# Kernel optimization log

Measured on AMD Instinct MI355X. Metric: run time of the kernel, lower is better.

Reference implementation:

```python
import jax, jax.numpy as jnp
import numpy as np

NUM_WIRES = 12
NUM_LAYERS = 3
BATCH = 8192
DIM = 2 ** NUM_WIRES


def _rx(theta):
    # RX(t) = [[cos(t/2), -i sin(t/2)], [-i sin(t/2), cos(t/2)]]; theta scalar or (B,)
    h = theta * 0.5
    c = jnp.cos(h).astype(jnp.complex64)
    s = (-1j) * jnp.sin(h).astype(jnp.complex64)
    return jnp.stack([jnp.stack([c, s], -1), jnp.stack([s, c], -1)], -2)


def _ry(theta):
    # RY(t) = [[cos(t/2), -sin(t/2)], [sin(t/2), cos(t/2)]]
    h = theta * 0.5
    c = jnp.cos(h)
    s = jnp.sin(h)
    m = jnp.stack([jnp.stack([c, -s], -1), jnp.stack([s, c], -1)], -2)
    return m.astype(jnp.complex64)


def _apply_1q(psi, mat, wire):
    # psi: (B, 2**n); pennylane wire 0 is most significant bit
    B = psi.shape[0]
    s = psi.reshape(B, 2 ** wire, 2, -1)
    if mat.ndim == 2:
        out = jnp.einsum('ij,bajc->baic', mat, s)
    else:  # per-sample gate, mat: (B, 2, 2)
        out = jnp.einsum('bij,bajc->baic', mat, s)
    return out.reshape(B, -1)


def _cnot(psi, control, target):
    B = psi.shape[0]
    a, b = (control, target) if control < target else (target, control)
    s = psi.reshape(B, 2 ** a, 2, 2 ** (b - a - 1), 2, -1)
    if control == a:
        # control on axis 2, flip target (axis 4) where control bit == 1
        s = s.at[:, :, 1].set(s[:, :, 1, :, ::-1])
    else:
        # control on axis 4, flip target (axis 2) where control bit == 1
        s = s.at[:, :, :, :, 1].set(s[:, :, ::-1, :, 1])
    return s.reshape(B, -1)


def _circuit(angles, weights):
    # angles: (B, n) per-sample input rotations; weights: (L, n, 2)
    B = angles.shape[0]
    n = NUM_WIRES
    psi = jnp.zeros((B, DIM), jnp.complex64).at[:, 0].set(1.0)
    for i in range(n):
        psi = _apply_1q(psi, _rx(angles[:, i]), i)
        psi = _apply_1q(psi, _ry(angles[:, i]), i)
    for l in range(NUM_LAYERS):
        for i in range(n):
            psi = _apply_1q(psi, _rx(weights[l, i, 0]), i)
            psi = _apply_1q(psi, _ry(weights[l, i, 1]), i)
        for i in range(n - 1):
            psi = _cnot(psi, i, i + 1)
        psi = _cnot(psi, n - 1, 0)
    probs = (psi.real ** 2 + psi.imag ** 2).reshape((B,) + (2,) * n)
    zs = []
    for i in range(n):
        other = tuple(j + 1 for j in range(n) if j != i)
        p = probs.sum(other)  # (B, 2)
        zs.append(p[:, 0] - p[:, 1])  # <Z_i> = P(0) - P(1)
    return jnp.stack(zs, -1)  # (B, n)


def setup_inputs() -> dict:
    key = jax.random.key(0)
    ks = jax.random.split(key, 5)
    return {
        'state_real': jax.random.normal(ks[0], (BATCH, DIM), jnp.float32),
        'state_imag': jax.random.normal(ks[1], (BATCH, DIM), jnp.float32),
        'weights': jax.random.normal(ks[2], (NUM_LAYERS, NUM_WIRES, 2), jnp.float32),
        'head_w': jax.random.normal(ks[3], (1, NUM_WIRES), jnp.float32) / np.sqrt(NUM_WIRES).astype(np.float32),
        'head_b': jax.random.normal(ks[4], (1,), jnp.float32),
    }


def reference(state_real, state_imag, weights, head_w, head_b):
    angles = jnp.arctan2(state_imag[:, :NUM_WIRES], state_real[:, :NUM_WIRES])  # (B, n)
    q = _circuit(angles, weights)  # (B, n)
    return (q @ head_w.T + head_b).squeeze(-1)  # (B,)
```

## Files before the change

### kernel.cpp

```cpp
#include <hip/hip_runtime.h>

typedef __fp16 h2v __attribute__((ext_vector_type(2)));
typedef _Float16 f16x8 __attribute__((ext_vector_type(8)));
typedef float f32x4 __attribute__((ext_vector_type(4)));

#define BLK 256
#define BATCH 8192

struct M12 { unsigned r[12]; };

constexpr M12 mp_matrix() {
  M12 m{};
  for (int p = 0; p <= 10; ++p) m.r[p] = (0xFFFu >> p) << p;
  m.r[11] = 0x7FFu;
  return m;
}
constexpr M12 MP = mp_matrix();

constexpr unsigned mv(const M12 m, unsigned v) {
  unsigned y = 0;
  for (int p = 0; p < 12; ++p)
    y |= (unsigned)(__builtin_popcount(m.r[p] & v) & 1) << p;
  return y;
}
constexpr M12 mmul(const M12 a, const M12 b) {
  M12 c{};
  for (int p = 0; p < 12; ++p) {
    unsigned acc = 0;
    for (int q = 0; q < 12; ++q)
      if ((a.r[p] >> q) & 1u) acc ^= b.r[q];
    c.r[p] = acc;
  }
  return c;
}
constexpr M12 minv(const M12 a0) {
  unsigned a[12] = {}, v[12] = {};
  for (int i = 0; i < 12; ++i) { a[i] = a0.r[i]; v[i] = 1u << i; }
  for (int c = 0; c < 12; ++c) {
    int piv = c;
    while (!((a[piv] >> c) & 1u)) ++piv;
    unsigned ta = a[piv], tv = v[piv];
    a[piv] = a[c]; v[piv] = v[c]; a[c] = ta; v[c] = tv;
    for (int r2 = 0; r2 < 12; ++r2)
      if (r2 != c && ((a[r2] >> c) & 1u)) { a[r2] ^= a[c]; v[r2] ^= v[c]; }
  }
  M12 out{};
  for (int i = 0; i < 12; ++i) out.r[i] = v[i];
  return out;
}
constexpr unsigned colq(const M12 m, int q) {
  unsigned c = 0;
  for (int p = 0; p < 12; ++p) c |= ((m.r[p] >> q) & 1u) << p;
  return c;
}
constexpr M12 from_cols(const unsigned (&c)[12]) {
  M12 m{};
  for (int p = 0; p < 12; ++p) {
    unsigned row = 0;
    for (int j = 0; j < 12; ++j) row |= ((c[j] >> p) & 1u) << j;
    m.r[p] = row;
  }
  return m;
}
constexpr M12 mk_id() { M12 m{}; for (int p = 0; p < 12; ++p) m.r[p] = 1u << p; return m; }
constexpr M12 MID = mk_id();
constexpr M12 MPI = minv(MP);

constexpr bool meq(const M12 a, const M12 b) {
  for (int p = 0; p < 12; ++p) if (a.r[p] != b.r[p]) return false;
  return true;
}
static_assert(meq(mmul(MP, MPI), MID), "P inverse");

struct Frame { M12 A, Ai; };
constexpr Frame FID{MID, MID};
constexpr Frame absorb(const Frame f) { return Frame{ mmul(MP, f.A), mmul(f.Ai, MPI) }; }
constexpr Frame apply_tau(const Frame f, const M12 t) {
  return Frame{ mmul(f.A, minv(t)), mmul(t, f.Ai) };
}

struct SSet { unsigned S[12]; };

constexpr int bankrank(const unsigned* v, int n) {
  unsigned basis[5] = {};
  int r = 0;
  for (int i = 0; i < n; ++i) {
    unsigned x = v[i] & 31u;
    for (int b = 4; b >= 0; --b) {
      if (!((x >> b) & 1u)) continue;
      if (basis[b]) x ^= basis[b];
      else { basis[b] = x; ++r; break; }
    }
  }
  return r;
}
constexpr bool ins_ech(unsigned (&e)[12], unsigned x) {
  for (int b = 11; b >= 0; --b) {
    if (!((x >> b) & 1u)) continue;
    if (e[b]) x ^= e[b];
    else { e[b] = x; return true; }
  }
  return false;
}
constexpr SSet build_S(const Frame f, const int* qs) {
  SSet s{};
  unsigned rows[4] = {};
  for (int i = 0; i < 4; ++i) {
    s.S[i] = colq(f.Ai, qs[i]);
    rows[i] = f.A.r[qs[i]];
  }
  unsigned R[4] = {rows[0], rows[1], rows[2], rows[3]};
  int pivcol[4] = {-1, -1, -1, -1};
  int nr = 0;
  for (int cc = 0; cc < 12 && nr < 4; ++cc) {
    int pr = -1;
    for (int r2 = nr; r2 < 4; ++r2) if ((R[r2] >> cc) & 1u) { pr = r2; break; }
    if (pr < 0) continue;
    unsigned tmp = R[nr]; R[nr] = R[pr]; R[pr] = tmp;
    for (int r2 = 0; r2 < 4; ++r2)
      if (r2 != nr && ((R[r2] >> cc) & 1u)) R[r2] ^= R[nr];
    pivcol[nr] = cc; ++nr;
  }
  unsigned nb[8] = {};
  int nc = 0;
  for (int j = 0; j < 12; ++j) {
    bool isp = false;
    for (int k = 0; k < nr; ++k) if (pivcol[k] == j) isp = true;
    if (isp) continue;
    unsigned v = 1u << j;
    for (int k = 0; k < nr; ++k) if ((R[k] >> j) & 1u) v |= 1u << pivcol[k];
    nb[nc] = v;
    ++nc;
  }
  unsigned pool[36] = {};
  int np = 0;
  for (int j = 0; j < 8; ++j) pool[np++] = nb[j];
  for (int j = 0; j < 8; ++j)
    for (int k = j + 1; k < 8; ++k) pool[np++] = nb[j] ^ nb[k];
  unsigned ech[12] = {};
  unsigned readset[5] = {};
  int nrs = 0;
  readset[nrs++] = s.S[0];
  for (int slot = 4; slot <= 7; ++slot) {
    int best = -1;
    unsigned bestc = 0;
    for (int c = 0; c < np; ++c) {
      unsigned tmp[12];
      for (int z = 0; z < 12; ++z) tmp[z] = ech[z];
      if (!ins_ech(tmp, pool[c])) continue;
      readset[nrs] = pool[c];
      const int rk = bankrank(readset, nrs + 1);
      if (rk > best) { best = rk; bestc = pool[c]; }
    }
    s.S[slot] = bestc;
    ins_ech(ech, bestc);
    readset[nrs++] = bestc;
  }
  const int rem[4] = {8, 9, 10, 11};
  for (int t = 0; t < 4; ++t) {
    for (int c = 0; c < np; ++c) {
      unsigned tmp[12];
      for (int z = 0; z < 12; ++z) tmp[z] = ech[z];
      if (!ins_ech(tmp, pool[c])) continue;
      s.S[rem[t]] = pool[c];
      ins_ech(ech, pool[c]);
      break;
    }
  }
  return s;
}
constexpr unsigned T4[4] = {8u, 4u, 2u, 1u};
constexpr M12 tau_of(const SSet s) {
  unsigned Sc[12], Dc[12];
  for (int i = 0; i < 12; ++i) {
    Sc[i] = s.S[i];
    Dc[i] = (i < 4) ? T4[i] : (1u << i);
  }
  return mmul(from_cols(Dc), minv(from_cols(Sc)));
}
constexpr int readrank_of(const SSet s) {
  unsigned v[5] = {s.S[0], s.S[4], s.S[5], s.S[6], s.S[7]};
  return bankrank(v, 5);
}
constexpr bool chk_group(const Frame f, const int* qs) {
  for (int i = 0; i < 4; ++i) if (colq(f.Ai, qs[i]) != T4[i]) return false;
  return true;
}

constexpr int QA[4] = {11, 10, 9, 8};
constexpr int QB[4] = {7, 6, 5, 4};
constexpr int QC[4] = {3, 2, 1, 0};

constexpr Frame F1  = absorb(FID);
constexpr SSet C0 = build_S(F1, QA);
constexpr M12  T0 = tau_of(C0);
constexpr Frame F2a = apply_tau(F1, T0);
constexpr SSet C1 = build_S(F2a, QB);
constexpr M12  T1 = tau_of(C1);
constexpr Frame F2b = apply_tau(F2a, T1);
constexpr SSet C2 = build_S(F2b, QC);
constexpr M12  T2 = tau_of(C2);
constexpr Frame F2c = apply_tau(F2b, T2);
constexpr Frame F3  = absorb(F2c);
constexpr SSet C3 = build_S(F3, QA);
constexpr M12  T3m = tau_of(C3);
constexpr Frame F3a = apply_tau(F3, T3m);
constexpr SSet C4 = build_S(F3a, QB);
constexpr M12  T4m = tau_of(C4);
constexpr Frame F3b = apply_tau(F3a, T4m);
constexpr SSet C5 = build_S(F3b, QC);
constexpr M12  T5m = tau_of(C5);
constexpr Frame F3c = apply_tau(F3b, T5m);
constexpr Frame F4  = absorb(F3c);

static_assert(chk_group(F2a, QA), "G2a");
static_assert(chk_group(F2b, QB), "G2b");
static_assert(chk_group(F2c, QC), "G2c");
static_assert(chk_group(F3a, QA), "G3a");
static_assert(chk_group(F3b, QB), "G3b");
static_assert(chk_group(F3c, QC), "G3c");
static_assert(F2a.A.r[11] == 8u && F2a.A.r[10] == 4u && F2a.A.r[9] == 2u && F2a.A.r[8] == 1u, "rows2a");
static_assert(F2b.A.r[7]  == 8u && F2b.A.r[6]  == 4u && F2b.A.r[5] == 2u && F2b.A.r[4] == 1u, "rows2b");
static_assert(F2c.A.r[3]  == 8u && F2c.A.r[2]  == 4u && F2c.A.r[1] == 2u && F2c.A.r[0] == 1u, "rows2c");
static_assert(F3a.A.r[11] == 8u && F3a.A.r[10] == 4u && F3a.A.r[9] == 2u && F3a.A.r[8] == 1u, "rows3a");
static_assert(F3b.A.r[7]  == 8u && F3b.A.r[6]  == 4u && F3b.A.r[5] == 2u && F3b.A.r[4] == 1u, "rows3b");
static_assert(F3c.A.r[3]  == 8u && F3c.A.r[2]  == 4u && F3c.A.r[1] == 2u && F3c.A.r[0] == 1u, "rows3c");
static_assert(readrank_of(C0) >= 3 && readrank_of(C1) >= 3 && readrank_of(C2) >= 3 &&
              readrank_of(C3) >= 3 && readrank_of(C4) >= 3 && readrank_of(C5) >= 3, "rr");

struct PT { unsigned rlb[5]; unsigned rwb[2]; unsigned ro[32]; };
constexpr PT mk_pt(const SSet s) {
  PT t{};
  t.rlb[0] = s.S[4]; t.rlb[1] = s.S[5]; t.rlb[2] = s.S[6]; t.rlb[3] = s.S[7];
  t.rlb[4] = s.S[0];
  t.rwb[0] = s.S[10]; t.rwb[1] = s.S[11];
  for (int m = 0; m < 4; ++m)
    for (int j = 0; j < 8; ++j)
      t.ro[(m << 3) | j] = ((m & 1) ? s.S[8] : 0u) ^ ((m & 2) ? s.S[9] : 0u) ^
                           ((j & 1) ? s.S[3] : 0u) ^ ((j & 2) ? s.S[2] : 0u) ^
                           ((j & 4) ? s.S[1] : 0u);
  return t;
}
constexpr PT RT[6] = { mk_pt(C0), mk_pt(C1), mk_pt(C2),
                       mk_pt(C3), mk_pt(C4), mk_pt(C5) };

template<int PI>
__device__ __forceinline__ unsigned rbase_of(const int lane, const int w) {
  unsigned rb = 0u;
  #pragma unroll
  for (int k = 0; k < 4; ++k) rb ^= ((lane >> k) & 1) ? RT[PI].rlb[k] : 0u;
  rb ^= ((lane >> 4) & 1) ? RT[PI].rlb[4] : 0u;
  rb ^= (w & 1) ? RT[PI].rwb[0] : 0u;
  rb ^= (w & 2) ? RT[PI].rwb[1] : 0u;
  return rb;
}

template<int PI>
__device__ __forceinline__ void do_pass(f32x4 (&D1)[4], f32x4 (&D2)[4],
                                        const unsigned* sb,
                                        const uint4 a1u, const uint4 a2u,
                                        const int lane, const int w,
                                        const unsigned sel) {
  const f16x8 A1f = __builtin_bit_cast(f16x8, a1u);
  const f16x8 A2f = __builtin_bit_cast(f16x8, a2u);
  const unsigned rb = rbase_of<PI>(lane, w);
  const f32x4 z4 = {0.f, 0.f, 0.f, 0.f};
  #pragma unroll
  for (int m = 0; m < 4; ++m) {
    unsigned amp[8];
    #pragma unroll
    for (int j = 0; j < 8; ++j)
      amp[j] = sb[rb ^ RT[PI].ro[(m << 3) | j]];
    uint4 bw;
    bw.x = __builtin_amdgcn_perm(amp[1], amp[0], sel);
    bw.y = __builtin_amdgcn_perm(amp[3], amp[2], sel);
    bw.z = __builtin_amdgcn_perm(amp[5], amp[4], sel);
    bw.w = __builtin_amdgcn_perm(amp[7], amp[6], sel);
    const f16x8 Bf = __builtin_bit_cast(f16x8, bw);
    D1[m] = __builtin_amdgcn_mfma_f32_16x16x32_f16(A1f, Bf, z4, 0, 0, 0);
    D2[m] = __builtin_amdgcn_mfma_f32_16x16x32_f16(A2f, Bf, z4, 0, 0, 0);
  }
}

__device__ __forceinline__ void write_state(const f32x4 (&D1)[4],
                                            const f32x4 (&D2)[4],
                                            unsigned* sb, const int lane,
                                            const int w) {
  const unsigned base = ((unsigned)w << 10) | ((unsigned)(lane & 15) << 4) |
                        ((unsigned)(lane >> 4) << 2);
  #pragma unroll
  for (int m = 0; m < 4; ++m) {
    uint4 v;
    v.x = __builtin_bit_cast(unsigned, __builtin_amdgcn_cvt_pkrtz(D1[m][0], D2[m][0]));
    v.y = __builtin_bit_cast(unsigned, __builtin_amdgcn_cvt_pkrtz(D1[m][1], D2[m][1]));
    v.z = __builtin_bit_cast(unsigned, __builtin_amdgcn_cvt_pkrtz(D1[m][2], D2[m][2]));
    v.w = __builtin_bit_cast(unsigned, __builtin_amdgcn_cvt_pkrtz(D1[m][3], D2[m][3]));
    *(uint4*)(sb + (base | ((unsigned)m << 8))) = v;
  }
}

__device__ __forceinline__ void gentry(const float4 g, const int rb,
                                       const int kb, float& re, float& im) {
  re = rb ? (kb ? g.x : g.z) : (kb ? -g.z : g.x);
  im = rb ? (kb ? -g.y : g.w) : (kb ? g.w : g.y);
}

__global__ __launch_bounds__(BLK) void amat_kernel(
    const float* __restrict__ wts, uint4* __restrict__ Am) {
  __shared__ float4 gt4[24];
  const int t = threadIdx.x;
  if (t < 24) {
    const int l = 1 + t / 12, i = t % 12;
    const float a  = wts[(l * 12 + i) * 2 + 0] * 0.5f;
    const float bb = wts[(l * 12 + i) * 2 + 1] * 0.5f;
    float sa, ca, sb2, cb;
    sincosf(a, &sa, &ca);
    sincosf(bb, &sb2, &cb);
    gt4[t] = make_float4(cb * ca, sb2 * sa, sb2 * ca, -cb * sa);
  }
  __syncthreads();
  #pragma unroll
  for (int rep = 0; rep < 3; ++rep) {
    const int idx = t + rep * BLK;
    const int pass = idx >> 7;
    const int mat  = (idx >> 6) & 1;
    const int lw   = idx & 63;
    const int r    = lw & 15;
    const int ks   = lw >> 4;
    const int imf  = ks >> 1;
    const float4 g0 = gt4[pass * 4 + 0];
    const float4 g1 = gt4[pass * 4 + 1];
    const float4 g2 = gt4[pass * 4 + 2];
    const float4 g3 = gt4[pass * 4 + 3];
    float b3r, b3i;
    gentry(g0, (r >> 3) & 1, ks & 1, b3r, b3i);
    float t2r[2], t2i[2];
    #pragma unroll
    for (int k2 = 0; k2 < 2; ++k2) {
      float cr, ci;
      gentry(g1, (r >> 2) & 1, k2, cr, ci);
      t2r[k2] = b3r * cr - b3i * ci;
      t2i[k2] = b3r * ci + b3i * cr;
    }
    float t1r[4], t1i[4];
    #pragma unroll
    for (int k2 = 0; k2 < 2; ++k2)
      #pragma unroll
      for (int k1 = 0; k1 < 2; ++k1) {
        float cr, ci;
        gentry(g2, (r >> 1) & 1, k1, cr, ci);
        t1r[k2 * 2 + k1] = t2r[k2] * cr - t2i[k2] * ci;
        t1i[k2 * 2 + k1] = t2r[k2] * ci + t2i[k2] * cr;
      }
    float ev[8];
    #pragma unroll
    for (int j = 0; j < 8; ++j) {
      float cr, ci;
      gentry(g3, r & 1, j & 1, cr, ci);
      const int h2 = j >> 1;
      const float er = t1r[h2] * cr - t1i[h2] * ci;
      const float ei = t1r[h2] * ci + t1i[h2] * cr;
      ev[j] = (mat == 0) ? (imf ? -ei : er) : (imf ? er : ei);
    }
    unsigned u[4];
    #pragma unroll
    for (int q = 0; q < 4; ++q) {
      const h2v pk = __builtin_amdgcn_cvt_pkrtz(ev[2 * q], ev[2 * q + 1]);
      u[q] = __builtin_bit_cast(unsigned, pk);
    }
    Am[(pass * 2 + mat) * 64 + lw] = make_uint4(u[0], u[1], u[2], u[3]);
  }
}

__global__ __launch_bounds__(BLK, 4) void qsim_kernel(
    const float* __restrict__ sr, const float* __restrict__ si,
    const float* __restrict__ wts, const float* __restrict__ hw,
    const float* __restrict__ hb, const uint4* __restrict__ Am,
    float* __restrict__ out) {
  __shared__ __align__(16) unsigned sbuf[2][4096];
  float4* qv = (float4*)(sbuf[1]);
  float* xacc = (float*)(sbuf[0]);

  const int t = threadIdx.x;
  const int lane = t & 63;
  const int w = t >> 6;
  const int s = blockIdx.x;

  uint4 A1u[6], A2u[6];
  #pragma unroll
  for (int p = 0; p < 6; ++p) {
    A1u[p] = Am[(p * 2 + 0) * 64 + lane];
    A2u[p] = Am[(p * 2 + 1) * 64 + lane];
  }

  if (t >= 64 && t < 76) {
    const int i = t - 64;
    const float ang = atan2f(si[(size_t)s * 4096 + i],
                             sr[(size_t)s * 4096 + i]) * 0.5f;
    float sn, cs;
    sincosf(ang, &sn, &cs);
    const float e0r = cs * cs, e0i = sn * sn, e1r = sn * cs, e1i = -sn * cs;
    const float a  = wts[i * 2 + 0] * 0.5f;
    const float bb = wts[i * 2 + 1] * 0.5f;
    float sa, ca, sb2, cb;
    sincosf(a, &sa, &ca);
    sincosf(bb, &sb2, &cb);
    const float g00r = cb * ca,  g00i = sb2 * sa, g01r = -sb2 * ca, g01i = -cb * sa;
    const float g10r = sb2 * ca, g10i = -cb * sa, g11r = cb * ca,   g11i = -sb2 * sa;
    const float q0r = g00r * e0r - g00i * e0i + g01r * e1r - g01i * e1i;
    const float q0i = g00r * e0i + g00i * e0r + g01r * e1i + g01i * e1r;
    const float q1r = g10r * e0r - g10i * e0i + g11r * e1r - g11i * e1i;
    const float q1i = g10r * e0i + g10i * e0r + g11r * e1i + g11i * e1r;
    qv[i] = make_float4(q0r, q0i, q1r, q1i);
  }
  __syncthreads();

  {
    const float4* q = qv;
    float Lr, Li;
    { const float4 q0 = q[0]; const int b0 = (w >> 1) & 1;
      Lr = b0 ? q0.z : q0.x; Li = b0 ? q0.w : q0.y; }
    { const float4 q1 = q[1]; const int b1 = w & 1;
      const float fr = b1 ? q1.z : q1.x, fi = b1 ? q1.w : q1.y;
      const float nr = Lr * fr - Li * fi, ni = Lr * fi + Li * fr;
      Lr = nr; Li = ni; }
    #pragma unroll
    for (int i = 2; i <= 7; ++i) {
      const float4 qq = q[i];
      const int bit = (lane >> (7 - i)) & 1;
      const float fr = bit ? qq.z : qq.x, fi = bit ? qq.w : qq.y;
      const float nr = Lr * fr - Li * fi, ni = Lr * fi + Li * fr;
      Lr = nr; Li = ni;
    }
    float LTr[4], LTi[4];
    { const float4 q8 = q[8], q9 = q[9];
      #pragma unroll
      for (int m = 0; m < 4; ++m) {
        const float xr2 = (m & 2) ? q8.z : q8.x, xi2 = (m & 2) ? q8.w : q8.y;
        const float yr = (m & 1) ? q9.z : q9.x, yi = (m & 1) ? q9.w : q9.y;
        const float tr = xr2 * yr - xi2 * yi, ti = xr2 * yi + xi2 * yr;
        LTr[m] = Lr * tr - Li * ti;
        LTi[m] = Lr * ti + Li * tr;
      } }
    float tbr[4], tbi[4];
    { const float4 qA = q[10], qB2 = q[11];
      #pragma unroll
      for (int m = 0; m < 4; ++m) {
        const float xr2 = (m & 2) ? qA.z : qA.x, xi2 = (m & 2) ? qA.w : qA.y;
        const float yr = (m & 1) ? qB2.z : qB2.x, yi = (m & 1) ? qB2.w : qB2.y;
        tbr[m] = xr2 * yr - xi2 * yi;
        tbi[m] = xr2 * yi + xi2 * yr;
      } }
    __syncthreads();
    const unsigned base = ((unsigned)w << 10) | ((unsigned)lane << 4);
    #pragma unroll
    for (int qq2 = 0; qq2 < 4; ++qq2) {
      uint4 v;
      unsigned* vp = &v.x;
      #pragma unroll
      for (int z = 0; z < 4; ++z) {
        const int l = qq2 * 4 + z;
        const float arl = LTr[l >> 2] * tbr[l & 3] - LTi[l >> 2] * tbi[l & 3];
        const float ail = LTr[l >> 2] * tbi[l & 3] + LTi[l >> 2] * tbr[l & 3];
        vp[z] = __builtin_bit_cast(unsigned, __builtin_amdgcn_cvt_pkrtz(arl, ail));
      }
      *(uint4*)(sbuf[0] + base + qq2 * 4) = v;
    }
  }
  __syncthreads();

  const unsigned sel = (lane & 32) ? 0x07060302u : 0x05040100u;
  f32x4 D1[4], D2[4];

  do_pass<0>(D1, D2, sbuf[0], A1u[0], A2u[0], lane, w, sel);
  write_state(D1, D2, sbuf[1], lane, w);
  __syncthreads();
  do_pass<1>(D1, D2, sbuf[1], A1u[1], A2u[1], lane, w, sel);
  write_state(D1, D2, sbuf[0], lane, w);
  __syncthreads();
  do_pass<2>(D1, D2, sbuf[0], A1u[2], A2u[2], lane, w, sel);
  write_state(D1, D2, sbuf[1], lane, w);
  __syncthreads();
  do_pass<3>(D1, D2, sbuf[1], A1u[3], A2u[3], lane, w, sel);
  write_state(D1, D2, sbuf[0], lane, w);
  __syncthreads();
  do_pass<4>(D1, D2, sbuf[0], A1u[4], A2u[4], lane, w, sel);
  write_state(D1, D2, sbuf[1], lane, w);
  __syncthreads();
  do_pass<5>(D1, D2, sbuf[1], A1u[5], A2u[5], lane, w, sel);

  const unsigned pbase = ((unsigned)w << 10) | ((unsigned)(lane & 15) << 4) |
                         ((unsigned)((lane >> 4) & 3) << 2);
  float hp[12];
  #pragma unroll
  for (int i = 0; i < 12; ++i) {
    const unsigned R = F4.A.r[11 - i];
    const float h = hw[i];
    hp[i] = (__popc(pbase & R & 0xCFCu) & 1) ? -h : h;
  }
  float c[16];
  #pragma unroll
  for (int v = 0; v < 16; ++v) c[v] = 0.f;
  #pragma unroll
  for (int i = 0; i < 12; ++i) {
    const unsigned R = F4.A.r[11 - i];
    const int mu = (int)((((R >> 8) & 3u) << 2) | (R & 3u));
    c[mu] += hp[i];
  }
  #pragma unroll
  for (int bb = 1; bb < 16; bb <<= 1)
    #pragma unroll
    for (int v = 0; v < 16; ++v)
      if (!(v & bb)) {
        const float x = c[v], y = c[v | bb];
        c[v] = x + y;
        c[v | bb] = x - y;
      }
  float acc = 0.f;
  #pragma unroll
  for (int m = 0; m < 4; ++m)
    #pragma unroll
    for (int r = 0; r < 4; ++r)
      acc += (D1[m][r] * D1[m][r] + D2[m][r] * D2[m][r]) * c[(m << 2) | r];
  #pragma unroll
  for (int off = 1; off < 64; off <<= 1) acc += __shfl_xor(acc, off, 64);

  __syncthreads();
  if (lane == 0) xacc[w] = acc;
  __syncthreads();
  if (t == 0) out[s] = xacc[0] + xacc[1] + xacc[2] + xacc[3] + hb[0];
}

extern "C" void kernel_launch(void* const* d_in, const int* in_sizes, int n_in,
                              void* d_out, int out_size, void* d_ws, size_t ws_size,
                              hipStream_t stream) {
  const float* sr  = (const float*)d_in[0];
  const float* si  = (const float*)d_in[1];
  const float* wts = (const float*)d_in[2];
  const float* hw  = (const float*)d_in[3];
  const float* hb  = (const float*)d_in[4];
  float* out = (float*)d_out;
  uint4* Am = (uint4*)d_ws;
  amat_kernel<<<1, BLK, 0, stream>>>(wts, Am);
  qsim_kernel<<<BATCH, BLK, 0, stream>>>(sr, si, wts, hw, hb, Am, out);
}
```

Before: 103.3 us.

## Add per-pass XOR bank swizzle to LDS state layout to cut conflicts

Introduces a compile-time searched XOR swizzle per pass that maps high address bits into bank-selecting bits, chosen to maximize the bank rank of the gather read pattern. Both writes of the state (initial fill and between passes) and the gathered reads apply the same swizzle, so each buffer is consistently permuted. The candidate selection for the basis also now prioritizes low-bit rank. The aim is fewer LDS bank conflicts in the strided amplitude gathers, at the cost of slightly more address XOR arithmetic.

```diff
diff --git a/kernel.cpp b/kernel.cpp
--- a/kernel.cpp
+++ b/kernel.cpp
@@ -81,11 +81,11 @@
 
 struct SSet { unsigned S[12]; };
 
-constexpr int bankrank(const unsigned* v, int n) {
+constexpr int rank_msk(const unsigned* v, int n, unsigned msk) {
   unsigned basis[5] = {};
   int r = 0;
   for (int i = 0; i < n; ++i) {
-    unsigned x = v[i] & 31u;
+    unsigned x = v[i] & msk;
     for (int b = 4; b >= 0; --b) {
       if (!((x >> b) & 1u)) continue;
       if (basis[b]) x ^= basis[b];
@@ -149,8 +149,9 @@
       for (int z = 0; z < 12; ++z) tmp[z] = ech[z];
       if (!ins_ech(tmp, pool[c])) continue;
       readset[nrs] = pool[c];
-      const int rk = bankrank(readset, nrs + 1);
-      if (rk > best) { best = rk; bestc = pool[c]; }
+      const int score = rank_msk(readset, nrs + 1, 3u) * 8 +
+                        rank_msk(readset, nrs + 1, 31u);
+      if (score > best) { best = score; bestc = pool[c]; }
     }
     s.S[slot] = bestc;
     ins_ech(ech, bestc);
@@ -178,13 +179,37 @@
   }
   return mmul(from_cols(Dc), minv(from_cols(Sc)));
 }
-constexpr int readrank_of(const SSet s) {
-  unsigned v[5] = {s.S[0], s.S[4], s.S[5], s.S[6], s.S[7]};
-  return bankrank(v, 5);
-}
 constexpr bool chk_group(const Frame f, const int* qs) {
   for (int i = 0; i < 4; ++i) if (colq(f.Ai, qs[i]) != T4[i]) return false;
   return true;
+}
+
+struct BSw { unsigned mk[7]; };
+constexpr unsigned bapp(const BSw& b, unsigned v) {
+  unsigned o = v;
+  for (int k = 0; k < 7; ++k)
+    if ((v >> (5 + k)) & 1u) o ^= b.mk[k];
+  return o;
+}
+constexpr int brank_read(const BSw& b, const SSet& s) {
+  unsigned v[5] = { bapp(b, s.S[0]), bapp(b, s.S[4]), bapp(b, s.S[5]),
+                    bapp(b, s.S[6]), bapp(b, s.S[7]) };
+  return rank_msk(v, 5, 31u);
+}
+constexpr BSw find_B(const SSet& s) {
+  BSw b{};
+  int best = brank_read(b, s);
+  for (int sw = 0; sw < 3; ++sw)
+    for (int k = 0; k < 7; ++k) {
+      unsigned bv = b.mk[k];
+      for (unsigned v = 0; v < 8; ++v) {
+        b.mk[k] = v << 2;
+        const int r = brank_read(b, s);
+        if (r > best) { best = r; bv = v << 2; }
+      }
+      b.mk[k] = bv;
+    }
+  return b;
 }
 
 constexpr int QA[4] = {11, 10, 9, 8};
@@ -225,24 +250,40 @@
 static_assert(F3a.A.r[11] == 8u && F3a.A.r[10] == 4u && F3a.A.r[9] == 2u && F3a.A.r[8] == 1u, "rows3a");
 static_assert(F3b.A.r[7]  == 8u && F3b.A.r[6]  == 4u && F3b.A.r[5] == 2u && F3b.A.r[4] == 1u, "rows3b");
 static_assert(F3c.A.r[3]  == 8u && F3c.A.r[2]  == 4u && F3c.A.r[1] == 2u && F3c.A.r[0] == 1u, "rows3c");
-static_assert(readrank_of(C0) >= 3 && readrank_of(C1) >= 3 && readrank_of(C2) >= 3 &&
-              readrank_of(C3) >= 3 && readrank_of(C4) >= 3 && readrank_of(C5) >= 3, "rr");
-
-struct PT { unsigned rlb[5]; unsigned rwb[2]; unsigned ro[32]; };
-constexpr PT mk_pt(const SSet s) {
+
+constexpr BSw B0 = find_B(C0);
+constexpr BSw B1 = find_B(C1);
+constexpr BSw B2 = find_B(C2);
+constexpr BSw B3 = find_B(C3);
+constexpr BSw B4 = find_B(C4);
+constexpr BSw B5 = find_B(C5);
+static_assert(brank_read(B0, C0) >= 3 && brank_read(B1, C1) >= 3 &&
+              brank_read(B2, C2) >= 3 && brank_read(B3, C3) >= 3 &&
+              brank_read(B4, C4) >= 3 && brank_read(B5, C5) >= 3, "rr");
+
+struct PT {
+  unsigned rlb[5]; unsigned rwb[2]; unsigned ro[32];
+  unsigned wlb[4]; unsigned wm[2]; unsigned wwb[2];
+};
+constexpr PT mk_pt(const SSet s, const BSw b) {
   PT t{};
-  t.rlb[0] = s.S[4]; t.rlb[1] = s.S[5]; t.rlb[2] = s.S[6]; t.rlb[3] = s.S[7];
-  t.rlb[4] = s.S[0];
-  t.rwb[0] = s.S[10]; t.rwb[1] = s.S[11];
+  t.rlb[0] = bapp(b, s.S[4]); t.rlb[1] = bapp(b, s.S[5]);
+  t.rlb[2] = bapp(b, s.S[6]); t.rlb[3] = bapp(b, s.S[7]);
+  t.rlb[4] = bapp(b, s.S[0]);
+  t.rwb[0] = bapp(b, s.S[10]); t.rwb[1] = bapp(b, s.S[11]);
   for (int m = 0; m < 4; ++m)
     for (int j = 0; j < 8; ++j)
-      t.ro[(m << 3) | j] = ((m & 1) ? s.S[8] : 0u) ^ ((m & 2) ? s.S[9] : 0u) ^
-                           ((j & 1) ? s.S[3] : 0u) ^ ((j & 2) ? s.S[2] : 0u) ^
-                           ((j & 4) ? s.S[1] : 0u);
+      t.ro[(m << 3) | j] = bapp(b,
+          ((m & 1) ? s.S[8] : 0u) ^ ((m & 2) ? s.S[9] : 0u) ^
+          ((j & 1) ? s.S[3] : 0u) ^ ((j & 2) ? s.S[2] : 0u) ^
+          ((j & 4) ? s.S[1] : 0u));
+  for (int k = 0; k < 4; ++k) t.wlb[k] = bapp(b, 1u << (4 + k));
+  t.wm[0] = bapp(b, 256u);  t.wm[1] = bapp(b, 512u);
+  t.wwb[0] = bapp(b, 1024u); t.wwb[1] = bapp(b, 2048u);
   return t;
 }
-constexpr PT RT[6] = { mk_pt(C0), mk_pt(C1), mk_pt(C2),
-                       mk_pt(C3), mk_pt(C4), mk_pt(C5) };
+constexpr PT RT[6] = { mk_pt(C0, B0), mk_pt(C1, B1), mk_pt(C2, B2),
+                       mk_pt(C3, B3), mk_pt(C4, B4), mk_pt(C5, B5) };
 
 template<int PI>
 __device__ __forceinline__ unsigned rbase_of(const int lane, const int w) {
@@ -282,20 +323,26 @@
   }
 }
 
+template<int PI>
 __device__ __forceinline__ void write_state(const f32x4 (&D1)[4],
                                             const f32x4 (&D2)[4],
                                             unsigned* sb, const int lane,
                                             const int w) {
-  const unsigned base = ((unsigned)w << 10) | ((unsigned)(lane & 15) << 4) |
-                        ((unsigned)(lane >> 4) << 2);
+  unsigned wb = (unsigned)((lane >> 4) << 2);
+  #pragma unroll
+  for (int k = 0; k < 4; ++k) wb ^= ((lane >> k) & 1) ? RT[PI].wlb[k] : 0u;
+  wb ^= (w & 1) ? RT[PI].wwb[0] : 0u;
+  wb ^= (w & 2) ? RT[PI].wwb[1] : 0u;
   #pragma unroll
   for (int m = 0; m < 4; ++m) {
+    const unsigned addr = wb ^ ((m & 1) ? RT[PI].wm[0] : 0u)
+                             ^ ((m & 2) ? RT[PI].wm[1] : 0u);
     uint4 v;
     v.x = __builtin_bit_cast(unsigned, __builtin_amdgcn_cvt_pkrtz(D1[m][0], D2[m][0]));
     v.y = __builtin_bit_cast(unsigned, __builtin_amdgcn_cvt_pkrtz(D1[m][1], D2[m][1]));
     v.z = __builtin_bit_cast(unsigned, __builtin_amdgcn_cvt_pkrtz(D1[m][2], D2[m][2]));
     v.w = __builtin_bit_cast(unsigned, __builtin_amdgcn_cvt_pkrtz(D1[m][3], D2[m][3]));
-    *(uint4*)(sb + (base | ((unsigned)m << 8))) = v;
+    *(uint4*)(sb + addr) = v;
   }
 }
 
@@ -452,7 +499,13 @@
         tbi[m] = xr2 * yi + xi2 * yr;
       } }
     __syncthreads();
-    const unsigned base = ((unsigned)w << 10) | ((unsigned)lane << 4);
+    unsigned wb = 0u;
+    #pragma unroll
+    for (int k = 0; k < 4; ++k) wb ^= ((lane >> k) & 1) ? RT[0].wlb[k] : 0u;
+    wb ^= (lane & 16) ? RT[0].wm[0] : 0u;
+    wb ^= (lane & 32) ? RT[0].wm[1] : 0u;
+    wb ^= (w & 1) ? RT[0].wwb[0] : 0u;
+    wb ^= (w & 2) ? RT[0].wwb[1] : 0u;
     #pragma unroll
     for (int qq2 = 0; qq2 < 4; ++qq2) {
       uint4 v;
@@ -464,7 +517,7 @@
         const float ail = LTr[l >> 2] * tbi[l & 3] + LTi[l >> 2] * tbr[l & 3];
         vp[z] = __builtin_bit_cast(unsigned, __builtin_amdgcn_cvt_pkrtz(arl, ail));
       }
-      *(uint4*)(sbuf[0] + base + qq2 * 4) = v;
+      *(uint4*)(sbuf[0] + (wb ^ ((unsigned)qq2 << 2))) = v;
     }
   }
   __syncthreads();
@@ -473,19 +526,19 @@
   f32x4 D1[4], D2[4];
 
   do_pass<0>(D1, D2, sbuf[0], A1u[0], A2u[0], lane, w, sel);
-  write_state(D1, D2, sbuf[1], lane, w);
+  write_state<1>(D1, D2, sbuf[1], lane, w);
   __syncthreads();
   do_pass<1>(D1, D2, sbuf[1], A1u[1], A2u[1], lane, w, sel);
-  write_state(D1, D2, sbuf[0], lane, w);
+  write_state<2>(D1, D2, sbuf[0], lane, w);
   __syncthreads();
   do_pass<2>(D1, D2, sbuf[0], A1u[2], A2u[2], lane, w, sel);
-  write_state(D1, D2, sbuf[1], lane, w);
+  write_state<3>(D1, D2, sbuf[1], lane, w);
   __syncthreads();
   do_pass<3>(D1, D2, sbuf[1], A1u[3], A2u[3], lane, w, sel);
-  write_state(D1, D2, sbuf[0], lane, w);
+  write_state<4>(D1, D2, sbuf[0], lane, w);
   __syncthreads();
   do_pass<4>(D1, D2, sbuf[0], A1u[4], A2u[4], lane, w, sel);
-  write_state(D1, D2, sbuf[1], lane, w);
+  write_state<5>(D1, D2, sbuf[1], lane, w);
   __syncthreads();
   do_pass<5>(D1, D2, sbuf[1], A1u[5], A2u[5], lane, w, sel);
 
```

Result: faster. 90.43 us (median of 2 runs) (-12.4%).
